# Kernel tuning notes

Hardware: AMD Instinct MI355X
Metric: run time of the kernel (lower is better)

## Reference

```python
import jax, jax.numpy as jnp
import numpy as np

DIM = 1024
HEADS = 16
HEAD_DIM = DIM // HEADS
HIDDEN = 4 * DIM
EPS = 1e-5


def layer_norm(x, g, b):
    mu = jnp.mean(x, axis=-1, keepdims=True)
    var = jnp.mean(jnp.square(x - mu), axis=-1, keepdims=True)
    return (x - mu) * jax.lax.rsqrt(var + EPS) * g + b


def fast_gelu(x):
    # Ascend fast_gelu == x * sigmoid(1.702 * x)
    return x * jax.nn.sigmoid(1.702 * x)


def setup_inputs() -> dict:
    key = jax.random.key(0)
    ks = jax.random.split(key, 12)
    B, N, C = 16, 577, DIM
    s_in = 1.0 / np.sqrt(DIM)
    s_hid = 1.0 / np.sqrt(HIDDEN)
    return {
        "x": jax.random.normal(ks[0], (B * N, C), jnp.float32),
        "norm1_g": jnp.ones((C,), jnp.float32),
        "norm1_b": jnp.zeros((C,), jnp.float32),
        "Wq": jax.random.normal(ks[1], (C, C), jnp.float32) * s_in,
        "Wk": jax.random.normal(ks[2], (C, C), jnp.float32) * s_in,
        "Wv": jax.random.normal(ks[3], (C, C), jnp.float32) * s_in,
        "Wp": jax.random.normal(ks[4], (C, C), jnp.float32) * s_in,
        "bp": jnp.zeros((C,), jnp.float32),
        "norm2_g": jnp.ones((C,), jnp.float32),
        "norm2_b": jnp.zeros((C,), jnp.float32),
        "W1": jax.random.normal(ks[5], (HIDDEN, C), jnp.float32) * s_in,
        "b1": jnp.zeros((HIDDEN,), jnp.float32),
        "W2": jax.random.normal(ks[6], (C, HIDDEN), jnp.float32) * s_hid,
        "b2": jnp.zeros((C,), jnp.float32),
        "B": B,
        "N": N,
        "C": C,
    }


def reference(x, norm1_g, norm1_b, Wq, Wk, Wv, Wp, bp, norm2_g, norm2_b, W1, b1, W2, b2, B, N, C):
    scale = HEAD_DIM ** -0.5

    h = layer_norm(x, norm1_g, norm1_b)          # [B*N, C]
    # qkv projections (qkv_bias=False), reshape to [B, H, N, D]
    def split_heads(y):
        return y.reshape(B, N, HEADS, HEAD_DIM).transpose(0, 2, 1, 3)

    q = split_heads(h @ Wq.T)
    k = split_heads(h @ Wk.T)
    v = split_heads(h @ Wv.T)

    attn = jnp.einsum('bhqd,bhkd->bhqk', q, k) * scale
    attn = jax.nn.softmax(attn, axis=-1)
    o = jnp.einsum('bhqk,bhkd->bhqd', attn, v)   # [B, H, N, D]
    o = o.transpose(0, 2, 1, 3).reshape(B * N, C)
    y = o @ Wp.T + bp                            # attention output proj

    x = x + y                                    # residual 1 (drop_path=0)
    h2 = layer_norm(x, norm2_g, norm2_b)
    m = fast_gelu(h2 @ W1.T + b1) @ W2.T + b2    # MLP (drop=0)
    return x + m                                 # residual 2
```

## Files before the change

### kernel.cpp

```cpp
#include <hip/hip_runtime.h>

typedef short  short8  __attribute__((ext_vector_type(8)));
typedef float  float4v __attribute__((ext_vector_type(4)));

#define DIM      1024
#define HEADS    16
#define HEAD_DIM 64
#define HIDDEN   4096
#define BATCH    16
#define SEQ      577
#define M_ROWS   (BATCH*SEQ)
#define NPAD2    640
#define QKVLD    3072
#define LOG2E    1.4426950408889634f

static __device__ __forceinline__ unsigned short f2bf(float f) {
  unsigned int u = __float_as_uint(f);
  u += 0x7FFFu + ((u >> 16) & 1u);
  return (unsigned short)(u >> 16);
}
static __device__ __forceinline__ float bf2f(unsigned short h) {
  return __uint_as_float(((unsigned int)h) << 16);
}
static __device__ __forceinline__ void gload_lds16(const void* g, void* l) {
  __builtin_amdgcn_global_load_lds(
      (const __attribute__((address_space(1))) void*)g,
      (__attribute__((address_space(3))) void*)l, 16, 0, 0);
}

__global__ __launch_bounds__(256) void f32_to_bf16_kernel(
    const float* __restrict__ in, unsigned short* __restrict__ out, int n4) {
  int i = blockIdx.x * 256 + threadIdx.x;
  if (i >= n4) return;
  float4 v = ((const float4*)in)[i];
  union { unsigned short s[4]; uint2 u; } p;
  p.s[0] = f2bf(v.x); p.s[1] = f2bf(v.y); p.s[2] = f2bf(v.z); p.s[3] = f2bf(v.w);
  ((uint2*)out)[i] = p.u;
}

__global__ __launch_bounds__(256) void ln_kernel(
    const float* __restrict__ x, const float* __restrict__ g,
    const float* __restrict__ b, unsigned short* __restrict__ out) {
  int row = blockIdx.x, tid = threadIdx.x;
  const float* xr = x + (long long)row * DIM;
  float4 v = *(const float4*)(xr + tid * 4);
  float s1 = v.x + v.y + v.z + v.w;
  float s2 = v.x*v.x + v.y*v.y + v.z*v.z + v.w*v.w;
  #pragma unroll
  for (int o = 32; o; o >>= 1) { s1 += __shfl_xor(s1, o); s2 += __shfl_xor(s2, o); }
  __shared__ float a1[4], a2[4];
  int wid = tid >> 6, lane = tid & 63;
  if (lane == 0) { a1[wid] = s1; a2[wid] = s2; }
  __syncthreads();
  s1 = a1[0] + a1[1] + a1[2] + a1[3];
  s2 = a2[0] + a2[1] + a2[2] + a2[3];
  float mean = s1 * (1.f / DIM);
  float var  = s2 * (1.f / DIM) - mean * mean;
  float rstd = rsqrtf(var + 1e-5f);
  float4 gv = *(const float4*)(g + tid * 4);
  float4 bv = *(const float4*)(b + tid * 4);
  union { unsigned short s[4]; uint2 u; } p;
  p.s[0] = f2bf((v.x - mean) * rstd * gv.x + bv.x);
  p.s[1] = f2bf((v.y - mean) * rstd * gv.y + bv.y);
  p.s[2] = f2bf((v.z - mean) * rstd * gv.z + bv.z);
  p.s[3] = f2bf((v.w - mean) * rstd * gv.w + bv.w);
  *(uint2*)(out + (long long)row * DIM + tid * 4) = p.u;
}

__global__ __launch_bounds__(256) void transpose_v_kernel(
    const unsigned short* __restrict__ v, unsigned short* __restrict__ vt) {
  int t = blockIdx.x * 256 + threadIdx.x;
  int chunk = t % 80;
  int rest  = t / 80;
  int d  = rest & 63;
  int bh = rest >> 6;
  int b = bh >> 4, h = bh & 15;
  union { unsigned short s[8]; uint4 u; } p;
  #pragma unroll
  for (int i = 0; i < 8; i++) {
    int n = chunk * 8 + i;
    p.s[i] = (n < SEQ) ? v[((long long)(b * SEQ + n)) * QKVLD + h * HEAD_DIM + d] : (unsigned short)0;
  }
  *(uint4*)(vt + ((long long)bh * HEAD_DIM + d) * NPAD2 + chunk * 8) = p.u;
}

template <bool MASK>
static __device__ __forceinline__ void attn_tile(
    const unsigned short* Ks, const unsigned short* Vs, unsigned short* Ps,
    const short8 (&af)[2][2], float4v (&oacc)[2][4], float4v (&sumacc)[2],
    int quad, int l16, int wid) {
  const float CE = 0.125f * LOG2E;

  short8 bfr[4][2];
  #pragma unroll
  for (int j = 0; j < 4; j++) {
    int r = j * 16 + l16;
    #pragma unroll
    for (int ks = 0; ks < 2; ks++)
      bfr[j][ks] = *(const short8*)(Ks + r * 64 + ((ks * 4 + quad) ^ (l16 & 7)) * 8);
  }

  float4v sacc[2][4];
  #pragma unroll
  for (int i = 0; i < 2; i++)
    #pragma unroll
    for (int j = 0; j < 4; j++) sacc[i][j] = (float4v){0.f, 0.f, 0.f, 0.f};
  #pragma unroll
  for (int i = 0; i < 2; i++)
    #pragma unroll
    for (int j = 0; j < 4; j++)
      #pragma unroll
      for (int ks = 0; ks < 2; ks++)
        sacc[i][j] = __builtin_amdgcn_mfma_f32_16x16x32_bf16(af[i][ks], bfr[j][ks], sacc[i][j], 0, 0, 0);

  #pragma unroll
  for (int i = 0; i < 2; i++) {
    #pragma unroll
    for (int reg = 0; reg < 4; reg++) {
      int prow = wid * 32 + i * 16 + quad * 4 + reg;
      #pragma unroll
      for (int j = 0; j < 4; j++) {
        float pv;
        if constexpr (MASK) {
          pv = (j == 0 && l16 == 0) ? __builtin_amdgcn_exp2f(sacc[i][j][reg] * CE) : 0.f;
        } else {
          pv = __builtin_amdgcn_exp2f(sacc[i][j][reg] * CE);
        }
        int pcol = j * 16 + l16;
        Ps[prow * 64 + (((pcol >> 3) ^ (prow & 7)) * 8) + (pcol & 7)] = f2bf(pv);
      }
    }
  }

  short8 paf[2][2], vbf[4][2];
  #pragma unroll
  for (int i = 0; i < 2; i++) {
    int r = wid * 32 + i * 16 + l16;
    #pragma unroll
    for (int kk = 0; kk < 2; kk++)
      paf[i][kk] = *(const short8*)(Ps + r * 64 + ((kk * 4 + quad) ^ (l16 & 7)) * 8);
  }
  #pragma unroll
  for (int j = 0; j < 4; j++) {
    int r = j * 16 + l16;
    #pragma unroll
    for (int kk = 0; kk < 2; kk++)
      vbf[j][kk] = *(const short8*)(Vs + r * 64 + ((kk * 4 + quad) ^ (l16 & 7)) * 8);
  }
  const short ov = (short)0x3F80;
  const short8 ones = (short8){ov, ov, ov, ov, ov, ov, ov, ov};
  #pragma unroll
  for (int i = 0; i < 2; i++) {
    #pragma unroll
    for (int kk = 0; kk < 2; kk++) {
      #pragma unroll
      for (int j = 0; j < 4; j++)
        oacc[i][j] = __builtin_amdgcn_mfma_f32_16x16x32_bf16(paf[i][kk], vbf[j][kk], oacc[i][j], 0, 0, 0);
      sumacc[i] = __builtin_amdgcn_mfma_f32_16x16x32_bf16(paf[i][kk], ones, sumacc[i], 0, 0, 0);
    }
  }
}

__global__ __launch_bounds__(256, 3) void flash_attn_kernel(
    const unsigned short* __restrict__ q,
    const unsigned short* __restrict__ k,
    const unsigned short* __restrict__ vt,
    unsigned short* __restrict__ o) {
  int qt = blockIdx.x;
  int bh = blockIdx.y;
  int b = bh >> 4, h = bh & 15;
  int q0 = qt * 128;
  int tid = threadIdx.x, lane = tid & 63, wid = tid >> 6;
  int quad = lane >> 4, l16 = lane & 15;
  long long rowbase = (long long)b * SEQ;

  __shared__ __align__(16) unsigned short SM[16384];
  unsigned short* Ks = SM;
  unsigned short* Vs = Ks + 64 * 64;
  unsigned short* Ps = Vs + 64 * 64;

  short8 af[2][2];
  #pragma unroll
  for (int i = 0; i < 2; i++) {
    int gr = q0 + wid * 32 + i * 16 + l16;
    if (gr > SEQ - 1) gr = SEQ - 1;
    const unsigned short* qr = q + (rowbase + gr) * QKVLD + h * HEAD_DIM;
    #pragma unroll
    for (int ks = 0; ks < 2; ks++)
      af[i][ks] = *(const short8*)(qr + (ks * 4 + quad) * 8);
  }

  float4v oacc[2][4];
  float4v sumacc[2];
  #pragma unroll
  for (int i = 0; i < 2; i++) {
    sumacc[i] = (float4v){0.f, 0.f, 0.f, 0.f};
    #pragma unroll
    for (int j = 0; j < 4; j++) oacc[i][j] = (float4v){0.f, 0.f, 0.f, 0.f};
  }

  for (int kt = 0; kt < 10; kt++) {
    if (kt) __syncthreads();
    #pragma unroll
    for (int p = 0; p < 2; p++) {
      int r = wid * 16 + p * 8 + (lane >> 3);
      int c = lane & 7;
      int gk = kt * 64 + r; if (gk > SEQ - 1) gk = SEQ - 1;
      gload_lds16(k + (rowbase + gk) * QKVLD + h * HEAD_DIM + ((c ^ (r & 7)) * 8),
                  Ks + (wid * 16 + p * 8) * 64);
      gload_lds16(vt + ((long long)bh * HEAD_DIM + r) * NPAD2 + kt * 64 + ((c ^ (r & 7)) * 8),
                  Vs + (wid * 16 + p * 8) * 64);
    }
    __syncthreads();
    if (kt < 9) attn_tile<false>(Ks, Vs, Ps, af, oacc, sumacc, quad, l16, wid);
    else        attn_tile<true >(Ks, Vs, Ps, af, oacc, sumacc, quad, l16, wid);
  }

  #pragma unroll
  for (int i = 0; i < 2; i++) {
    #pragma unroll
    for (int reg = 0; reg < 4; reg++) {
      int grow = q0 + wid * 32 + i * 16 + quad * 4 + reg;
      if (grow >= SEQ) continue;
      float inv = 1.f / sumacc[i][reg];
      #pragma unroll
      for (int j = 0; j < 4; j++) {
        int d = j * 16 + l16;
        o[(rowbase + grow) * DIM + h * HEAD_DIM + d] = f2bf(oacc[i][j][reg] * inv);
      }
    }
  }
}

enum { EPI_BF16 = 0, EPI_BIAS_RES_F32 = 2, EPI_BIAS_GELU_BF16 = 3 };

template <int EPI>
__global__ __launch_bounds__(256, 2) void gemm_nt(
    const unsigned short* __restrict__ A, int lda,
    const unsigned short* __restrict__ B, int ldb,
    void* __restrict__ Cout, int ldc,
    const float* __restrict__ bias, const float* __restrict__ res,
    int M, int N, int K) {
  int mt = gridDim.x, nt = gridDim.y;
  int id = blockIdx.y * mt + blockIdx.x;
  int band  = id / (8 * nt);
  int rem   = id - band * 8 * nt;
  int mrem  = mt - band * 8;
  int bandh = mrem < 8 ? mrem : 8;
  int lm = rem % bandh;
  int nb = rem / bandh;
  int m0 = (band * 8 + lm) * 128, n0 = nb * 128;

  int tid = threadIdx.x;
  int lane = tid & 63, wid = tid >> 6;
  int wm = wid >> 1, wn = wid & 1;
  int quad = lane >> 4, l16 = lane & 15;

  __shared__ __align__(16) char SMEM[32768];
  unsigned short* As = (unsigned short*)SMEM;
  unsigned short* Bs = As + 128 * 64;

  float4v acc[4][4];
  #pragma unroll
  for (int i = 0; i < 4; i++)
    #pragma unroll
    for (int j = 0; j < 4; j++) acc[i][j] = (float4v){0.f, 0.f, 0.f, 0.f};

  int lr8 = lane >> 3;
  int lc8 = lane & 7;
  int sc  = (lc8 ^ lr8) * 8;

  for (int k0 = 0; k0 < K; k0 += 64) {
    #pragma unroll
    for (int p = 0; p < 4; p++) {
      int ra = wid * 32 + p * 8;
      int gr = m0 + ra + lr8; if (gr > M - 1) gr = M - 1;
      gload_lds16(A + (long long)gr * lda + k0 + sc, As + ra * 64);
      int gn = n0 + ra + lr8; if (gn > N - 1) gn = N - 1;
      gload_lds16(B + (long long)gn * ldb + k0 + sc, Bs + ra * 64);
    }
    __syncthreads();
    #pragma unroll
    for (int ks = 0; ks < 2; ks++) {
      short8 af[4], bfr[4];
      #pragma unroll
      for (int i = 0; i < 4; i++)
        af[i]  = *(const short8*)(As + (wm * 64 + i * 16 + l16) * 64 + (((ks * 4 + quad) ^ (l16 & 7)) * 8));
      #pragma unroll
      for (int j = 0; j < 4; j++)
        bfr[j] = *(const short8*)(Bs + (wn * 64 + j * 16 + l16) * 64 + (((ks * 4 + quad) ^ (l16 & 7)) * 8));
      #pragma unroll
      for (int i = 0; i < 4; i++)
        #pragma unroll
        for (int j = 0; j < 4; j++)
          acc[i][j] = __builtin_amdgcn_mfma_f32_16x16x32_bf16(af[i], bfr[j], acc[i][j], 0, 0, 0);
    }
    __syncthreads();
  }

  float* cs = (float*)SMEM + wid * (16 * 68);
  int erow = lane >> 2;
  int eq   = lane & 3;

  #pragma unroll
  for (int i = 0; i < 4; i++) {
    #pragma unroll
    for (int j = 0; j < 4; j++)
      #pragma unroll
      for (int r = 0; r < 4; r++)
        cs[(quad * 4 + r) * 68 + j * 16 + l16] = acc[i][j][r];
    int grow = m0 + wm * 64 + i * 16 + erow;
    bool rowok = grow < M;

    if constexpr (EPI == EPI_BIAS_RES_F32) {
      #pragma unroll
      for (int t = 0; t < 4; t++) {
        int colb = t * 16 + eq * 4;
        int gcol = n0 + wn * 64 + colb;
        if (!rowok || gcol >= N) continue;
        float4 vv = *(const float4*)&cs[erow * 68 + colb];
        float4 bb = *(const float4*)&bias[gcol];
        const float4 rr = *(const float4*)&res[(long long)grow * ldc + gcol];
        vv.x += bb.x + rr.x; vv.y += bb.y + rr.y;
        vv.z += bb.z + rr.z; vv.w += bb.w + rr.w;
        *(float4*)((float*)Cout + (long long)grow * ldc + gcol) = vv;
      }
    } else {
      #pragma unroll
      for (int h = 0; h < 2; h++) {
        int colb = h * 32 + eq * 8;
        int gcol = n0 + wn * 64 + colb;
        if (!rowok || gcol >= N) continue;
        float4 a0 = *(const float4*)&cs[erow * 68 + colb];
        float4 a1 = *(const float4*)&cs[erow * 68 + colb + 4];
        float vs[8] = {a0.x, a0.y, a0.z, a0.w, a1.x, a1.y, a1.z, a1.w};
        if constexpr (EPI == EPI_BIAS_GELU_BF16) {
          float4 b0 = *(const float4*)&bias[gcol];
          float4 b1 = *(const float4*)&bias[gcol + 4];
          float bs[8] = {b0.x, b0.y, b0.z, b0.w, b1.x, b1.y, b1.z, b1.w};
          #pragma unroll
          for (int e = 0; e < 8; e++) {
            float tt = vs[e] + bs[e];
            float ex = __builtin_amdgcn_exp2f(tt * -2.4554669595930156f);
            vs[e] = tt / (1.f + ex);
          }
        }
        union { unsigned short s[8]; uint4 u; } p;
        #pragma unroll
        for (int e = 0; e < 8; e++) p.s[e] = f2bf(vs[e]);
        *(uint4*)((unsigned short*)Cout + (long long)grow * ldc + gcol) = p.u;
      }
    }
  }
}

extern "C" void kernel_launch(void* const* d_in, const int* in_sizes, int n_in,
                              void* d_out, int out_size, void* d_ws, size_t ws_size,
                              hipStream_t stream) {
  const float* x   = (const float*)d_in[0];
  const float* g1  = (const float*)d_in[1];
  const float* be1 = (const float*)d_in[2];
  const float* Wq  = (const float*)d_in[3];
  const float* Wk  = (const float*)d_in[4];
  const float* Wv  = (const float*)d_in[5];
  const float* Wp  = (const float*)d_in[6];
  const float* bp  = (const float*)d_in[7];
  const float* g2  = (const float*)d_in[8];
  const float* be2 = (const float*)d_in[9];
  const float* W1  = (const float*)d_in[10];
  const float* b1  = (const float*)d_in[11];
  const float* W2  = (const float*)d_in[12];
  const float* b2  = (const float*)d_in[13];
  float* out = (float*)d_out;

  char* ws = (char*)d_ws;
  size_t off = 0;
  auto alloc = [&](size_t bytes) {
    size_t r = off; off += (bytes + 255) & ~(size_t)255; return r;
  };
  unsigned short* wqkv_bf = (unsigned short*)(ws + alloc((size_t)3 * DIM * DIM * 2));
  unsigned short* wp_bf   = (unsigned short*)(ws + alloc((size_t)DIM * DIM * 2));
  unsigned short* w1_bf   = (unsigned short*)(ws + alloc((size_t)HIDDEN * DIM * 2));
  unsigned short* w2_bf   = (unsigned short*)(ws + alloc((size_t)HIDDEN * DIM * 2));
  unsigned short* h_bf    = (unsigned short*)(ws + alloc((size_t)M_ROWS * DIM * 2));
  unsigned short* qkv_bf  = (unsigned short*)(ws + alloc((size_t)M_ROWS * QKVLD * 2));
  unsigned short* vt_bf   = (unsigned short*)(ws + alloc((size_t)256 * HEAD_DIM * NPAD2 * 2));

  unsigned short* o_bf  = h_bf;
  unsigned short* h2_bf = h_bf;
  unsigned short* u_bf  = qkv_bf;
  float*          x1    = out;

  f32_to_bf16_kernel<<<DIM * DIM / 4 / 256, 256, 0, stream>>>(Wq, wqkv_bf, DIM * DIM / 4);
  f32_to_bf16_kernel<<<DIM * DIM / 4 / 256, 256, 0, stream>>>(Wk, wqkv_bf + DIM * DIM, DIM * DIM / 4);
  f32_to_bf16_kernel<<<DIM * DIM / 4 / 256, 256, 0, stream>>>(Wv, wqkv_bf + 2 * DIM * DIM, DIM * DIM / 4);
  f32_to_bf16_kernel<<<DIM * DIM / 4 / 256, 256, 0, stream>>>(Wp, wp_bf, DIM * DIM / 4);
  f32_to_bf16_kernel<<<HIDDEN * DIM / 4 / 256, 256, 0, stream>>>(W1, w1_bf, HIDDEN * DIM / 4);
  f32_to_bf16_kernel<<<HIDDEN * DIM / 4 / 256, 256, 0, stream>>>(W2, w2_bf, HIDDEN * DIM / 4);

  ln_kernel<<<M_ROWS, 256, 0, stream>>>(x, g1, be1, h_bf);

  gemm_nt<EPI_BF16><<<dim3(73, 24), 256, 0, stream>>>(h_bf, DIM, wqkv_bf, DIM,
      qkv_bf, QKVLD, nullptr, nullptr, M_ROWS, 3 * DIM, DIM);

  transpose_v_kernel<<<256 * HEAD_DIM * (NPAD2 / 8) / 256, 256, 0, stream>>>(
      qkv_bf + 2 * DIM, vt_bf);

  flash_attn_kernel<<<dim3(5, 256), 256, 0, stream>>>(
      qkv_bf, qkv_bf + DIM, vt_bf, o_bf);

  gemm_nt<EPI_BIAS_RES_F32><<<dim3(73, 8), 256, 0, stream>>>(o_bf, DIM, wp_bf, DIM,
      x1, DIM, bp, x, M_ROWS, DIM, DIM);

  ln_kernel<<<M_ROWS, 256, 0, stream>>>(x1, g2, be2, h2_bf);

  gemm_nt<EPI_BIAS_GELU_BF16><<<dim3(73, 32), 256, 0, stream>>>(h2_bf, DIM, w1_bf, DIM,
      u_bf, HIDDEN, b1, nullptr, M_ROWS, HIDDEN, DIM);

  gemm_nt<EPI_BIAS_RES_F32><<<dim3(73, 8), 256, 0, stream>>>(u_bf, HIDDEN, w2_bf, HIDDEN,
      out, DIM, b2, x1, M_ROWS, DIM, HIDDEN);
}
```

Baseline: 593.4 us.

## Double-buffer GEMM and attention K/V staging, fuse weight casts, tile V transpose

The GEMM and flash-attention kernels now keep two LDS buffers, so the next K tile is loaded while the current one is computed. This replaces the two __syncthreads per iteration with a single waitcnt plus barrier. The six weight-conversion launches become one combined kernel, and the V transpose now goes through an LDS tile so global reads and writes are coalesced. Doubling LDS to 64KB in the GEMM (and 48KB in attention) may reduce occupancy.

```diff
diff --git a/kernel.cpp b/kernel.cpp
--- a/kernel.cpp
+++ b/kernel.cpp
@@ -19,23 +19,32 @@
   u += 0x7FFFu + ((u >> 16) & 1u);
   return (unsigned short)(u >> 16);
 }
-static __device__ __forceinline__ float bf2f(unsigned short h) {
-  return __uint_as_float(((unsigned int)h) << 16);
-}
 static __device__ __forceinline__ void gload_lds16(const void* g, void* l) {
   __builtin_amdgcn_global_load_lds(
       (const __attribute__((address_space(1))) void*)g,
       (__attribute__((address_space(3))) void*)l, 16, 0, 0);
 }
 
-__global__ __launch_bounds__(256) void f32_to_bf16_kernel(
-    const float* __restrict__ in, unsigned short* __restrict__ out, int n4) {
+__global__ __launch_bounds__(256) void convert_all_kernel(
+    const float* __restrict__ Wq, const float* __restrict__ Wk,
+    const float* __restrict__ Wv, const float* __restrict__ Wp,
+    const float* __restrict__ W1, const float* __restrict__ W2,
+    unsigned short* __restrict__ wqkv, unsigned short* __restrict__ wp,
+    unsigned short* __restrict__ w1, unsigned short* __restrict__ w2) {
+  const int S = DIM * DIM / 4;
   int i = blockIdx.x * 256 + threadIdx.x;
-  if (i >= n4) return;
-  float4 v = ((const float4*)in)[i];
+  const float* src; unsigned short* dst; int rel;
+  if (i < 4 * S) {
+    if (i < S)        { src = Wq; dst = wqkv;               rel = i; }
+    else if (i < 2*S) { src = Wk; dst = wqkv + DIM * DIM;   rel = i - S; }
+    else if (i < 3*S) { src = Wv; dst = wqkv + 2*DIM*DIM;   rel = i - 2*S; }
+    else              { src = Wp; dst = wp;                 rel = i - 3*S; }
+  } else if (i < 8*S) { src = W1; dst = w1;                 rel = i - 4*S; }
+  else                { src = W2; dst = w2;                 rel = i - 8*S; }
+  float4 v = ((const float4*)src)[rel];
   union { unsigned short s[4]; uint2 u; } p;
   p.s[0] = f2bf(v.x); p.s[1] = f2bf(v.y); p.s[2] = f2bf(v.z); p.s[3] = f2bf(v.w);
-  ((uint2*)out)[i] = p.u;
+  ((uint2*)dst)[rel] = p.u;
 }
 
 __global__ __launch_bounds__(256) void ln_kernel(
@@ -69,19 +78,31 @@
 
 __global__ __launch_bounds__(256) void transpose_v_kernel(
     const unsigned short* __restrict__ v, unsigned short* __restrict__ vt) {
-  int t = blockIdx.x * 256 + threadIdx.x;
-  int chunk = t % 80;
-  int rest  = t / 80;
-  int d  = rest & 63;
-  int bh = rest >> 6;
+  int nt0 = blockIdx.x * 64;
+  int bh = blockIdx.y;
   int b = bh >> 4, h = bh & 15;
-  union { unsigned short s[8]; uint4 u; } p;
-  #pragma unroll
-  for (int i = 0; i < 8; i++) {
-    int n = chunk * 8 + i;
-    p.s[i] = (n < SEQ) ? v[((long long)(b * SEQ + n)) * QKVLD + h * HEAD_DIM + d] : (unsigned short)0;
-  }
-  *(uint4*)(vt + ((long long)bh * HEAD_DIM + d) * NPAD2 + chunk * 8) = p.u;
+  __shared__ unsigned short T[64][72];
+  int tid = threadIdx.x;
+  int r = tid >> 3;
+  int c = tid & 7;
+  #pragma unroll
+  for (int p = 0; p < 2; p++) {
+    int row = p * 32 + r;
+    int n = nt0 + row;
+    uint4 val = (uint4){0u, 0u, 0u, 0u};
+    if (n < SEQ)
+      val = *(const uint4*)(v + ((long long)(b * SEQ + n)) * QKVLD + h * HEAD_DIM + c * 8);
+    *(uint4*)&T[row][c * 8] = val;
+  }
+  __syncthreads();
+  #pragma unroll
+  for (int p = 0; p < 2; p++) {
+    int d = p * 32 + (tid >> 3);
+    union { unsigned short s[8]; uint4 u; } o;
+    #pragma unroll
+    for (int i = 0; i < 8; i++) o.s[i] = T[c * 8 + i][d];
+    *(uint4*)(vt + ((long long)bh * HEAD_DIM + d) * NPAD2 + nt0 + c * 8) = o.u;
+  }
 }
 
 template <bool MASK>
@@ -174,46 +195,58 @@
   int quad = lane >> 4, l16 = lane & 15;
   long long rowbase = (long long)b * SEQ;
 
-  __shared__ __align__(16) unsigned short SM[16384];
-  unsigned short* Ks = SM;
-  unsigned short* Vs = Ks + 64 * 64;
-  unsigned short* Ps = Vs + 64 * 64;
-
-  short8 af[2][2];
-  #pragma unroll
-  for (int i = 0; i < 2; i++) {
-    int gr = q0 + wid * 32 + i * 16 + l16;
-    if (gr > SEQ - 1) gr = SEQ - 1;
-    const unsigned short* qr = q + (rowbase + gr) * QKVLD + h * HEAD_DIM;
-    #pragma unroll
-    for (int ks = 0; ks < 2; ks++)
-      af[i][ks] = *(const short8*)(qr + (ks * 4 + quad) * 8);
-  }
-
-  float4v oacc[2][4];
-  float4v sumacc[2];
-  #pragma unroll
-  for (int i = 0; i < 2; i++) {
-    sumacc[i] = (float4v){0.f, 0.f, 0.f, 0.f};
-    #pragma unroll
-    for (int j = 0; j < 4; j++) oacc[i][j] = (float4v){0.f, 0.f, 0.f, 0.f};
-  }
-
-  for (int kt = 0; kt < 10; kt++) {
-    if (kt) __syncthreads();
+  __shared__ __align__(16) unsigned short SM[24576];
+  unsigned short* Ps = SM + 16384;
+
+  auto stageKV = [&](int sel, int kt) {
+    unsigned short* Ks_ = SM + sel * 8192;
+    unsigned short* Vs_ = Ks_ + 4096;
     #pragma unroll
     for (int p = 0; p < 2; p++) {
       int r = wid * 16 + p * 8 + (lane >> 3);
       int c = lane & 7;
       int gk = kt * 64 + r; if (gk > SEQ - 1) gk = SEQ - 1;
       gload_lds16(k + (rowbase + gk) * QKVLD + h * HEAD_DIM + ((c ^ (r & 7)) * 8),
-                  Ks + (wid * 16 + p * 8) * 64);
+                  Ks_ + (wid * 16 + p * 8) * 64);
       gload_lds16(vt + ((long long)bh * HEAD_DIM + r) * NPAD2 + kt * 64 + ((c ^ (r & 7)) * 8),
-                  Vs + (wid * 16 + p * 8) * 64);
-    }
-    __syncthreads();
-    if (kt < 9) attn_tile<false>(Ks, Vs, Ps, af, oacc, sumacc, quad, l16, wid);
-    else        attn_tile<true >(Ks, Vs, Ps, af, oacc, sumacc, quad, l16, wid);
+                  Vs_ + (wid * 16 + p * 8) * 64);
+    }
+  };
+
+  short8 af[2][2];
+  #pragma unroll
+  for (int i = 0; i < 2; i++) {
+    int gr = q0 + wid * 32 + i * 16 + l16;
+    if (gr > SEQ - 1) gr = SEQ - 1;
+    const unsigned short* qr = q + (rowbase + gr) * QKVLD + h * HEAD_DIM;
+    #pragma unroll
+    for (int ks = 0; ks < 2; ks++)
+      af[i][ks] = *(const short8*)(qr + (ks * 4 + quad) * 8);
+  }
+
+  float4v oacc[2][4];
+  float4v sumacc[2];
+  #pragma unroll
+  for (int i = 0; i < 2; i++) {
+    sumacc[i] = (float4v){0.f, 0.f, 0.f, 0.f};
+    #pragma unroll
+    for (int j = 0; j < 4; j++) oacc[i][j] = (float4v){0.f, 0.f, 0.f, 0.f};
+  }
+
+  stageKV(0, 0);
+  asm volatile("s_waitcnt vmcnt(0)" ::: "memory");
+  __builtin_amdgcn_s_barrier();
+
+  for (int kt = 0; kt < 10; kt++) {
+    int cur = kt & 1;
+    if (kt < 9) stageKV(cur ^ 1, kt + 1);
+    const unsigned short* Ks_ = SM + cur * 8192;
+    const unsigned short* Vs_ = Ks_ + 4096;
+    if (kt < 9) attn_tile<false>(Ks_, Vs_, Ps, af, oacc, sumacc, quad, l16, wid);
+    else        attn_tile<true >(Ks_, Vs_, Ps, af, oacc, sumacc, quad, l16, wid);
+    __builtin_amdgcn_sched_barrier(0);
+    asm volatile("s_waitcnt vmcnt(0)" ::: "memory");
+    __builtin_amdgcn_s_barrier();
   }
 
   #pragma unroll
@@ -256,9 +289,7 @@
   int wm = wid >> 1, wn = wid & 1;
   int quad = lane >> 4, l16 = lane & 15;
 
-  __shared__ __align__(16) char SMEM[32768];
-  unsigned short* As = (unsigned short*)SMEM;
-  unsigned short* Bs = As + 128 * 64;
+  __shared__ __align__(16) char SMEM[65536];
 
   float4v acc[4][4];
   #pragma unroll
@@ -270,32 +301,47 @@
   int lc8 = lane & 7;
   int sc  = (lc8 ^ lr8) * 8;
 
-  for (int k0 = 0; k0 < K; k0 += 64) {
+  auto stage = [&](int sel, int k0) {
+    unsigned short* As_ = (unsigned short*)SMEM + sel * (2 * 128 * 64);
+    unsigned short* Bs_ = As_ + 128 * 64;
     #pragma unroll
     for (int p = 0; p < 4; p++) {
       int ra = wid * 32 + p * 8;
       int gr = m0 + ra + lr8; if (gr > M - 1) gr = M - 1;
-      gload_lds16(A + (long long)gr * lda + k0 + sc, As + ra * 64);
+      gload_lds16(A + (long long)gr * lda + k0 + sc, As_ + ra * 64);
       int gn = n0 + ra + lr8; if (gn > N - 1) gn = N - 1;
-      gload_lds16(B + (long long)gn * ldb + k0 + sc, Bs + ra * 64);
-    }
-    __syncthreads();
+      gload_lds16(B + (long long)gn * ldb + k0 + sc, Bs_ + ra * 64);
+    }
+  };
+
+  int T = K >> 6;
+  stage(0, 0);
+  asm volatile("s_waitcnt vmcnt(0)" ::: "memory");
+  __builtin_amdgcn_s_barrier();
+
+  for (int t = 0; t < T; t++) {
+    int cur = t & 1;
+    if (t + 1 < T) stage(cur ^ 1, (t + 1) << 6);
+    const unsigned short* As_ = (const unsigned short*)SMEM + cur * (2 * 128 * 64);
+    const unsigned short* Bs_ = As_ + 128 * 64;
     #pragma unroll
     for (int ks = 0; ks < 2; ks++) {
       short8 af[4], bfr[4];
       #pragma unroll
       for (int i = 0; i < 4; i++)
-        af[i]  = *(const short8*)(As + (wm * 64 + i * 16 + l16) * 64 + (((ks * 4 + quad) ^ (l16 & 7)) * 8));
+        af[i]  = *(const short8*)(As_ + (wm * 64 + i * 16 + l16) * 64 + (((ks * 4 + quad) ^ (l16 & 7)) * 8));
       #pragma unroll
       for (int j = 0; j < 4; j++)
-        bfr[j] = *(const short8*)(Bs + (wn * 64 + j * 16 + l16) * 64 + (((ks * 4 + quad) ^ (l16 & 7)) * 8));
+        bfr[j] = *(const short8*)(Bs_ + (wn * 64 + j * 16 + l16) * 64 + (((ks * 4 + quad) ^ (l16 & 7)) * 8));
       #pragma unroll
       for (int i = 0; i < 4; i++)
         #pragma unroll
         for (int j = 0; j < 4; j++)
           acc[i][j] = __builtin_amdgcn_mfma_f32_16x16x32_bf16(af[i], bfr[j], acc[i][j], 0, 0, 0);
     }
-    __syncthreads();
+    __builtin_amdgcn_sched_barrier(0);
+    asm volatile("s_waitcnt vmcnt(0)" ::: "memory");
+    __builtin_amdgcn_s_barrier();
   }
 
   float* cs = (float*)SMEM + wid * (16 * 68);
@@ -391,20 +437,15 @@
   unsigned short* u_bf  = qkv_bf;
   float*          x1    = out;
 
-  f32_to_bf16_kernel<<<DIM * DIM / 4 / 256, 256, 0, stream>>>(Wq, wqkv_bf, DIM * DIM / 4);
-  f32_to_bf16_kernel<<<DIM * DIM / 4 / 256, 256, 0, stream>>>(Wk, wqkv_bf + DIM * DIM, DIM * DIM / 4);
-  f32_to_bf16_kernel<<<DIM * DIM / 4 / 256, 256, 0, stream>>>(Wv, wqkv_bf + 2 * DIM * DIM, DIM * DIM / 4);
-  f32_to_bf16_kernel<<<DIM * DIM / 4 / 256, 256, 0, stream>>>(Wp, wp_bf, DIM * DIM / 4);
-  f32_to_bf16_kernel<<<HIDDEN * DIM / 4 / 256, 256, 0, stream>>>(W1, w1_bf, HIDDEN * DIM / 4);
-  f32_to_bf16_kernel<<<HIDDEN * DIM / 4 / 256, 256, 0, stream>>>(W2, w2_bf, HIDDEN * DIM / 4);
+  convert_all_kernel<<<12 * (DIM * DIM / 4) / 256, 256, 0, stream>>>(
+      Wq, Wk, Wv, Wp, W1, W2, wqkv_bf, wp_bf, w1_bf, w2_bf);
 
   ln_kernel<<<M_ROWS, 256, 0, stream>>>(x, g1, be1, h_bf);
 
   gemm_nt<EPI_BF16><<<dim3(73, 24), 256, 0, stream>>>(h_bf, DIM, wqkv_bf, DIM,
       qkv_bf, QKVLD, nullptr, nullptr, M_ROWS, 3 * DIM, DIM);
 
-  transpose_v_kernel<<<256 * HEAD_DIM * (NPAD2 / 8) / 256, 256, 0, stream>>>(
-      qkv_bf + 2 * DIM, vt_bf);
+  transpose_v_kernel<<<dim3(10, 256), 256, 0, stream>>>(qkv_bf + 2 * DIM, vt_bf);
 
   flash_attn_kernel<<<dim3(5, 256), 256, 0, stream>>>(
       qkv_bf, qkv_bf + DIM, vt_bf, o_bf);
```

After: 539.5 us. 1.1x faster.
